# Performance work log

Hardware: AMD Instinct MI355X
Metric: run time of the kernel (lower is better)

## Reference

```python
import jax, jax.numpy as jnp
import numpy as np
import math

N_VERT = 35709
N_FACE = 70789
BATCH = 32


def _normalize(x, axis=-1, eps=1e-12):
    n = jnp.linalg.norm(x, axis=axis, keepdims=True)
    return x / jnp.maximum(n, eps)


def setup_inputs() -> dict:
    key = jax.random.key(0)
    ks = jax.random.split(key, 9)
    coeff = jax.random.normal(ks[0], (BATCH, 277), jnp.float32)
    idBase = jax.random.normal(ks[1], (3 * N_VERT, 80), jnp.float32)
    exBase = jax.random.normal(ks[2], (3 * N_VERT, 64), jnp.float32)
    texBase = jax.random.normal(ks[3], (3 * N_VERT, 100), jnp.float32)
    meanshape = jax.random.normal(ks[4], (3 * N_VERT,), jnp.float32)
    meantex = jax.random.normal(ks[5], (3 * N_VERT,), jnp.float32)
    face_buf = jax.random.randint(ks[6], (N_FACE, 3), 0, N_VERT, jnp.int32)
    # point_buf may index the appended zero-normal row at position N_FACE (padding)
    point_buf = jax.random.randint(ks[7], (N_VERT, 8), 0, N_FACE + 1, jnp.int32)
    keypoints = jax.random.randint(ks[8], (68,), 0, N_VERT, jnp.int32)
    return dict(coeff=coeff, idBase=idBase, exBase=exBase, texBase=texBase,
                meanshape=meanshape, meantex=meantex, face_buf=face_buf,
                point_buf=point_buf, keypoints=keypoints)


def reference(coeff, idBase, exBase, texBase, meanshape, meantex,
              face_buf, point_buf, keypoints):
    B = coeff.shape[0]
    # ---- Split_coeff (canonical 80/64/100/3/27/3 layout) ----
    id_c = coeff[:, :80]
    ex_c = coeff[:, 80:144]
    tex_c = coeff[:, 144:244]
    angles = coeff[:, 244:247]
    gamma = coeff[:, 247:274]
    trans = coeff[:, 274:277]
    cam_scale = jnp.ones((B, 1), coeff.dtype)
    f_scale = jnp.ones((B, 1), coeff.dtype)

    # ---- Shape formation ----
    fs = (jnp.einsum('ij,aj->ai', idBase, id_c)
          + jnp.einsum('ij,aj->ai', exBase, ex_c)
          + meanshape[None, :])
    fs = fs.reshape(B, -1, 3)  # [B, N, 3]
    fs = fs - jnp.mean(meanshape.reshape(-1, 3), axis=0)[None, None, :]

    # ---- Texture formation ----
    tex = (jnp.einsum('ij,aj->ai', texBase, tex_c) + meantex[None, :]).reshape(B, -1, 3)

    # ---- Rotation matrix (Rz @ Ry @ Rx, then transpose) ----
    cx, sx = jnp.cos(angles[:, 0]), jnp.sin(angles[:, 0])
    cy, sy = jnp.cos(angles[:, 1]), jnp.sin(angles[:, 1])
    cz, sz = jnp.cos(angles[:, 2]), jnp.sin(angles[:, 2])
    o, z = jnp.ones_like(cx), jnp.zeros_like(cx)
    Rx = jnp.stack([o, z, z, z, cx, -sx, z, sx, cx], -1).reshape(B, 3, 3)
    Ry = jnp.stack([cy, z, sy, z, o, z, -sy, z, cy], -1).reshape(B, 3, 3)
    Rz = jnp.stack([cz, -sz, z, sz, cz, z, z, z, o], -1).reshape(B, 3, 3)
    rot = jnp.swapaxes(jnp.matmul(jnp.matmul(Rz, Ry), Rx), 1, 2)  # [B,3,3]

    # ---- Compute_norm: gather face verts, cross, aggregate to vertices ----
    v1 = fs[:, face_buf[:, 0], :]  # [B, F, 3]
    v2 = fs[:, face_buf[:, 1], :]
    v3 = fs[:, face_buf[:, 2], :]
    face_norm = _normalize(jnp.cross(v1 - v2, v2 - v3), axis=2)  # [B, F, 3]
    face_norm = jnp.concatenate(
        [face_norm, jnp.zeros((B, 1, 3), face_norm.dtype)], axis=1)  # pad row
    v_norm = _normalize(jnp.sum(face_norm[:, point_buf, :], axis=2), axis=2)  # [B,N,3]

    norm_r = jnp.matmul(v_norm, rot)

    # ---- Rigid transform + landmarks ----
    fst = jnp.matmul(fs, rot) + trans[:, None, :]
    lm = fst[:, keypoints, :]  # [B, 68, 3]

    # ---- Projection block (applied to landmarks) ----
    focal = 1015.0 * f_scale  # [B,1]
    camera_pos = jnp.array([0.0, 0.0, 10.0], coeff.dtype) * cam_scale[:, :, None]  # [B,1,3]
    reverse_z = jnp.diag(jnp.array([1.0, 1.0, -1.0], coeff.dtype))
    z1 = jnp.zeros((B, 1), coeff.dtype)
    z2 = jnp.zeros((B, 2), coeff.dtype)
    o1 = jnp.ones((B, 1), coeff.dtype)
    p_matrix = jnp.concatenate(
        [focal, z1, 112.0 * o1, z1, focal, 112.0 * o1, z2, o1], axis=1).reshape(B, 3, 3)
    lm_cam = jnp.matmul(lm, reverse_z[None]) + camera_pos
    aug = jnp.matmul(lm_cam, jnp.swapaxes(p_matrix, 1, 2))
    landmark_p = aug[..., :2] / aug[..., 2:3]

    # ---- SH illumination ----
    init_lit = jnp.array([0.8, 0, 0, 0, 0, 0, 0, 0, 0], coeff.dtype)
    g = gamma.reshape(B, 3, 9) + init_lit[None, None, :]
    pi = math.pi
    a0, a1, a2 = pi, 2 * pi / math.sqrt(3.0), 2 * pi / math.sqrt(8.0)
    c0 = 1.0 / math.sqrt(4 * pi)
    c1 = math.sqrt(3.0) / math.sqrt(4 * pi)
    c2 = 3 * math.sqrt(5.0) / math.sqrt(12 * pi)
    nx, ny, nz = norm_r[..., 0], norm_r[..., 1], norm_r[..., 2]
    Y = jnp.stack([
        a0 * c0 * jnp.ones_like(nx),
        -a1 * c1 * ny,
        a1 * c1 * nz,
        -a1 * c1 * nx,
        a2 * c2 * nx * ny,
        -a2 * c2 * ny * nz,
        a2 * c2 * 0.5 / math.sqrt(3.0) * (3 * nz * nz - 1),
        -a2 * c2 * nx * nz,
        a2 * c2 * 0.5 * (nx * nx - ny * ny),
    ], axis=-1)  # [B, N, 9]
    lighting = jnp.einsum('bnk,bck->bnc', Y, g)  # [B, N, 3]
    face_color = tex * lighting

    return face_color, landmark_p, fst
```

## Files before the change

### kernel.cpp

```cpp
#include <hip/hip_runtime.h>

#define N_VERT 35709
#define N_FACE 70789
#define NB 32
#define M3 (3*N_VERT)

#define WS_FS4X  ((size_t)0)
#define WS_FN4X  (WS_FS4X + (size_t)N_VERT*128)
#define WS_CPAD  (WS_FN4X + (size_t)(N_FACE+1)*128)
#define WS_ROT   (WS_CPAD + (size_t)NB*256)
#define WS_TRE   (WS_ROT + (size_t)NB*9)
#define WS_G     (WS_TRE + (size_t)NB*3)
#define WS_MEAN  (WS_G + (size_t)NB*27)

#define FC_OFF   ((size_t)0)
#define LM_OFF   ((size_t)NB*M3)
#define FST_OFF  (LM_OFF + (size_t)NB*68*2)

#define A0C0 0.88622692545275801f
#define A1C1 1.77245385090551603f
#define A2C2 2.42703239430f
#define Y6C  0.70062393935f
#define Y8C  1.21351619715f

__global__ void __launch_bounds__(256) face3d_stageA1(
    const float* __restrict__ ms, float* __restrict__ ws) {
  float s0=0.f, s1=0.f, s2=0.f;
  for (int v = blockIdx.x*256 + threadIdx.x; v < N_VERT; v += gridDim.x*256) {
    s0 += ms[3*v+0]; s1 += ms[3*v+1]; s2 += ms[3*v+2];
  }
  #pragma unroll
  for (int off = 32; off > 0; off >>= 1) {
    s0 += __shfl_down(s0, off);
    s1 += __shfl_down(s1, off);
    s2 += __shfl_down(s2, off);
  }
  if ((threadIdx.x & 63) == 0) {
    atomicAdd(&ws[WS_MEAN+0], s0);
    atomicAdd(&ws[WS_MEAN+1], s1);
    atomicAdd(&ws[WS_MEAN+2], s2);
  }
}

__global__ void __launch_bounds__(256) face3d_stageA2(
    const float* __restrict__ coeff, float* __restrict__ ws) {
  int t = threadIdx.x;
  float m0 = ws[WS_MEAN+0]*(1.0f/N_VERT);
  float m1 = ws[WS_MEAN+1]*(1.0f/N_VERT);
  float m2 = ws[WS_MEAN+2]*(1.0f/N_VERT);
  float4* cp4 = (float4*)(ws + WS_CPAD);
  for (int idx = t; idx < 64*32; idx += 256) {
    int s4 = idx >> 5, b = idx & 31;
    int k = 4*s4;
    float4 v;
    v.x = (k < 244) ? coeff[b*277 + k + 0] : 0.f;
    v.y = (k < 244) ? coeff[b*277 + k + 1] : 0.f;
    v.z = (k < 244) ? coeff[b*277 + k + 2] : 0.f;
    v.w = (k < 244) ? coeff[b*277 + k + 3] : 0.f;
    cp4[idx] = v;
  }
  for (int idx = t; idx < NB*27; idx += 256) {
    int b = idx / 27, k = idx - b*27;
    ws[WS_G + idx] = coeff[b*277 + 247 + k] + (((k % 9) == 0) ? 0.8f : 0.0f);
  }
  if (t < NB) {
    int b = t;
    float ax = coeff[b*277+244], ay = coeff[b*277+245], az = coeff[b*277+246];
    float cx=cosf(ax), sx=sinf(ax);
    float cy=cosf(ay), sy=sinf(ay);
    float cz=cosf(az), sz=sinf(az);
    float T00=cz*cy, T01=-sz, T02=cz*sy;
    float T10=sz*cy, T11=cz,  T12=sz*sy;
    float T20=-sy,   T21=0.f, T22=cy;
    float R[3][3];
    R[0][0]=T00; R[0][1]=T01*cx+T02*sx; R[0][2]=-T01*sx+T02*cx;
    R[1][0]=T10; R[1][1]=T11*cx+T12*sx; R[1][2]=-T11*sx+T12*cx;
    R[2][0]=T20; R[2][1]=T21*cx+T22*sx; R[2][2]=-T21*sx+T22*cx;
    float rot[3][3];
    #pragma unroll
    for (int c=0;c<3;c++)
      #pragma unroll
      for (int j=0;j<3;j++)
        rot[c][j] = R[j][c];
    #pragma unroll
    for (int c=0;c<3;c++)
      #pragma unroll
      for (int j=0;j<3;j++)
        ws[WS_ROT + b*9 + c*3 + j] = rot[c][j];
    #pragma unroll
    for (int j=0;j<3;j++)
      ws[WS_TRE + b*3 + j] = coeff[b*277+274+j]
        - (m0*rot[0][j] + m1*rot[1][j] + m2*rot[2][j]);
  }
}


template<int NK4, int SOFF>
__device__ __forceinline__ void phaseKs(const float4* __restrict__ A,
                                        const float4* __restrict__ W,
                                        float* __restrict__ acc) {
  float4 cur = A[0];
  #pragma unroll 1
  for (int s = 0; s < NK4; ++s) {
    float4 a = cur;
    if (s + 1 < NK4) cur = A[s+1];
    const float4* __restrict__ Ws = W + (size_t)(SOFF + s)*32;
    #pragma unroll
    for (int b = 0; b < NB; ++b) {
      float4 w = Ws[b];
      acc[b] = fmaf(a.w, w.w, fmaf(a.z, w.z, fmaf(a.y, w.y, fmaf(a.x, w.x, acc[b]))));
    }
  }
}

__global__ void __launch_bounds__(256) face3d_stageB(
    const float* __restrict__ idB, const float* __restrict__ exB,
    const float* __restrict__ texB, const float* __restrict__ meanshape,
    const float* __restrict__ meantex, const float* __restrict__ cpadT,
    float* __restrict__ fs4x, float* __restrict__ texOut) {
  int t = threadIdx.x;
  int bid = blockIdx.x;
  int isTex = bid & 1;
  int r = (bid >> 1)*256 + t;
  if (r >= M3) return;
  const float4* __restrict__ W = (const float4*)cpadT;

  float acc[NB];
  #pragma unroll
  for (int b = 0; b < NB; ++b) acc[b] = 0.f;

  if (!isTex) {
    phaseKs<20, 0 >((const float4*)idB + (size_t)r*20, W, acc);
    phaseKs<16, 20>((const float4*)exB + (size_t)r*16, W, acc);
    float msv = meanshape[r];
    int v = r/3, c = r - 3*v;
    float* dst = fs4x + (size_t)v*128 + c;
    #pragma unroll
    for (int b = 0; b < NB; ++b) dst[b*4] = acc[b] + msv;
  } else {
    phaseKs<25, 36>((const float4*)texB + (size_t)r*25, W, acc);
    float mtv = meantex[r];
    #pragma unroll
    for (int b = 0; b < NB; ++b) texOut[(size_t)b*M3 + r] = acc[b] + mtv;
  }
}

__global__ void __launch_bounds__(256) face3d_stageC(
    const int* __restrict__ face_buf, const float* __restrict__ fs4x,
    float* __restrict__ fn4x) {
  int t = threadIdx.x;
  int b = t & 31, fi = t >> 5;
  int f = blockIdx.x*8 + fi;
  if (f > N_FACE) return;
  float4* o = (float4*)(fn4x + ((size_t)f*32 + b)*4);
  if (f == N_FACE) { *o = make_float4(0.f,0.f,0.f,0.f); return; }
  int i0 = face_buf[f*3+0];
  int i1 = face_buf[f*3+1];
  int i2 = face_buf[f*3+2];
  float4 p1 = *(const float4*)(fs4x + ((size_t)i0*32 + b)*4);
  float4 p2 = *(const float4*)(fs4x + ((size_t)i1*32 + b)*4);
  float4 p3 = *(const float4*)(fs4x + ((size_t)i2*32 + b)*4);
  float e1x = p1.x-p2.x, e1y = p1.y-p2.y, e1z = p1.z-p2.z;
  float e2x = p2.x-p3.x, e2y = p2.y-p3.y, e2z = p2.z-p3.z;
  float nx = e1y*e2z - e1z*e2y;
  float ny = e1z*e2x - e1x*e2z;
  float nz = e1x*e2y - e1y*e2x;
  float inv = 1.0f / fmaxf(sqrtf(nx*nx + ny*ny + nz*nz), 1e-12f);
  *o = make_float4(nx*inv, ny*inv, nz*inv, 0.f);
}

__global__ void __launch_bounds__(256) face3d_stageD(
    const int* __restrict__ point_buf, const int* __restrict__ keypoints,
    const float* __restrict__ fs4x, const float* __restrict__ fn4x,
    const float* __restrict__ rotAll, const float* __restrict__ treAll,
    const float* __restrict__ gAll, float* __restrict__ out) {
  const int mainBlocks = (N_VERT + 7)/8;
  int bid = blockIdx.x;
  int t = threadIdx.x;
  if (bid < mainBlocks) {
    __shared__ float rotL[NB*9];
    __shared__ float treL[NB*3];
    __shared__ float gL[NB*27];
    __shared__ float fstL[NB*33];
    __shared__ float LL[NB*33];
    if (t < NB*9)  rotL[t] = rotAll[t];
    if (t < NB*3)  treL[t] = treAll[t];
    for (int i = t; i < NB*27; i += 256) gL[i] = gAll[i];
    __syncthreads();
    int b = t & 31, vi = t >> 5;
    int v0 = bid*8;
    int v = v0 + vi;
    if (v < N_VERT) {
      const int4 pb0 = *(const int4*)(point_buf + (size_t)v*8);
      const int4 pb1 = *(const int4*)(point_buf + (size_t)v*8 + 4);
      float4 g0 = *(const float4*)(fn4x + ((size_t)pb0.x*32 + b)*4);
      float4 g1 = *(const float4*)(fn4x + ((size_t)pb0.y*32 + b)*4);
      float4 g2 = *(const float4*)(fn4x + ((size_t)pb0.z*32 + b)*4);
      float4 g3 = *(const float4*)(fn4x + ((size_t)pb0.w*32 + b)*4);
      float4 g4 = *(const float4*)(fn4x + ((size_t)pb1.x*32 + b)*4);
      float4 g5 = *(const float4*)(fn4x + ((size_t)pb1.y*32 + b)*4);
      float4 g6 = *(const float4*)(fn4x + ((size_t)pb1.z*32 + b)*4);
      float4 g7 = *(const float4*)(fn4x + ((size_t)pb1.w*32 + b)*4);
      float sx = ((g0.x+g1.x)+(g2.x+g3.x)) + ((g4.x+g5.x)+(g6.x+g7.x));
      float sy = ((g0.y+g1.y)+(g2.y+g3.y)) + ((g4.y+g5.y)+(g6.y+g7.y));
      float sz = ((g0.z+g1.z)+(g2.z+g3.z)) + ((g4.z+g5.z)+(g6.z+g7.z));
      float inv = 1.0f / fmaxf(sqrtf(sx*sx + sy*sy + sz*sz), 1e-12f);
      float n0 = sx*inv, n1 = sy*inv, n2 = sz*inv;
      const float* rot = rotL + b*9;
      float r00=rot[0], r01=rot[1], r02=rot[2];
      float r10=rot[3], r11=rot[4], r12=rot[5];
      float r20=rot[6], r21=rot[7], r22=rot[8];
      float nx = n0*r00 + n1*r10 + n2*r20;
      float ny = n0*r01 + n1*r11 + n2*r21;
      float nz = n0*r02 + n1*r12 + n2*r22;
      float Y1 = -A1C1*ny;
      float Y2 =  A1C1*nz;
      float Y3 = -A1C1*nx;
      float Y4 =  A2C2*nx*ny;
      float Y5 = -A2C2*ny*nz;
      float Y6 =  Y6C*(3.f*nz*nz - 1.f);
      float Y7 = -A2C2*nx*nz;
      float Y8 =  Y8C*(nx*nx - ny*ny);
      const float* g = gL + b*27;
      #pragma unroll
      for (int c = 0; c < 3; ++c) {
        const float* gc = g + c*9;
        float Lc = A0C0*gc[0] + Y1*gc[1] + Y2*gc[2] + Y3*gc[3] + Y4*gc[4]
                 + Y5*gc[5] + Y6*gc[6] + Y7*gc[7] + Y8*gc[8];
        LL[b*33 + vi*4 + c] = Lc;
      }
      float4 fsv = *(const float4*)(fs4x + ((size_t)v*32 + b)*4);
      const float* tre = treL + b*3;
      fstL[b*33 + vi*4 + 0] = fsv.x*r00 + fsv.y*r10 + fsv.z*r20 + tre[0];
      fstL[b*33 + vi*4 + 1] = fsv.x*r01 + fsv.y*r11 + fsv.z*r21 + tre[1];
      fstL[b*33 + vi*4 + 2] = fsv.x*r02 + fsv.y*r12 + fsv.z*r22 + tre[2];
    }
    __syncthreads();
    int b2 = t >> 3, w = t & 7;
    if (v0 + w < N_VERT) {
      size_t obase = (size_t)b2*M3 + (size_t)(v0 + w)*3;
      float f0 = fstL[b2*33 + w*4 + 0];
      float f1 = fstL[b2*33 + w*4 + 1];
      float f2 = fstL[b2*33 + w*4 + 2];
      out[FST_OFF + obase + 0] = f0;
      out[FST_OFF + obase + 1] = f1;
      out[FST_OFF + obase + 2] = f2;
      float l0 = LL[b2*33 + w*4 + 0];
      float l1 = LL[b2*33 + w*4 + 1];
      float l2 = LL[b2*33 + w*4 + 2];
      float t0 = out[FC_OFF + obase + 0];
      float t1 = out[FC_OFF + obase + 1];
      float t2 = out[FC_OFF + obase + 2];
      out[FC_OFF + obase + 0] = t0*l0;
      out[FC_OFF + obase + 1] = t1*l1;
      out[FC_OFF + obase + 2] = t2*l2;
    }
  } else {
    int idx = (bid - mainBlocks)*256 + t;
    if (idx >= NB*68) return;
    int b = idx & 31, j = idx >> 5;
    int kp = keypoints[j];
    const float* rot = rotAll + b*9;
    const float* tre = treAll + b*3;
    float4 fsv = *(const float4*)(fs4x + ((size_t)kp*32 + b)*4);
    float o0 = fsv.x*rot[0] + fsv.y*rot[3] + fsv.z*rot[6] + tre[0];
    float o1 = fsv.x*rot[1] + fsv.y*rot[4] + fsv.z*rot[7] + tre[1];
    float o2 = fsv.x*rot[2] + fsv.y*rot[5] + fsv.z*rot[8] + tre[2];
    float zc = 10.0f - o2;
    float axv = 1015.0f*o0 + 112.0f*zc;
    float ayv = 1015.0f*o1 + 112.0f*zc;
    out[LM_OFF + (size_t)b*136 + (size_t)j*2 + 0] = axv/zc;
    out[LM_OFF + (size_t)b*136 + (size_t)j*2 + 1] = ayv/zc;
  }
}

extern "C" void kernel_launch(void* const* d_in, const int* in_sizes, int n_in,
                              void* d_out, int out_size, void* d_ws, size_t ws_size,
                              hipStream_t stream) {
  const float* coeff     = (const float*)d_in[0];
  const float* idB       = (const float*)d_in[1];
  const float* exB       = (const float*)d_in[2];
  const float* texB      = (const float*)d_in[3];
  const float* meanshape = (const float*)d_in[4];
  const float* meantex   = (const float*)d_in[5];
  const int*   face_buf  = (const int*)d_in[6];
  const int*   point_buf = (const int*)d_in[7];
  const int*   keypoints = (const int*)d_in[8];
  float* out = (float*)d_out;
  float* ws  = (float*)d_ws;

  hipMemsetAsync((char*)d_ws + WS_MEAN*sizeof(float), 0, 3*sizeof(float), stream);

  hipLaunchKernelGGL(face3d_stageA1, dim3(56), dim3(256), 0, stream, meanshape, ws);
  hipLaunchKernelGGL(face3d_stageA2, dim3(1), dim3(256), 0, stream, coeff, ws);

  int gridB = 2 * ((M3 + 255)/256);
  hipLaunchKernelGGL(face3d_stageB, dim3(gridB), dim3(256), 0, stream,
                     idB, exB, texB, meanshape, meantex,
                     ws + WS_CPAD, ws + WS_FS4X, out + FC_OFF);

  int gridC = (N_FACE + 1 + 7)/8;
  hipLaunchKernelGGL(face3d_stageC, dim3(gridC), dim3(256), 0, stream,
                     face_buf, ws + WS_FS4X, ws + WS_FN4X);

  int mainBlocks = (N_VERT + 7)/8;
  int lmBlocks   = (NB*68 + 255)/256;
  hipLaunchKernelGGL(face3d_stageD, dim3(mainBlocks + lmBlocks), dim3(256), 0, stream,
                     point_buf, keypoints, ws + WS_FS4X, ws + WS_FN4X,
                     ws + WS_ROT, ws + WS_TRE, ws + WS_G, out);
}
```

Measured before the change: 291.5 us.

## Stage coefficient weights in LDS and compute two rows per thread in stageB

The basis GEMM kernel now copies the per-batch coefficient matrix into shared memory once per block. Each thread computes two output rows, so every loaded weight float4 feeds twice as many FMAs. Blocks shrink to 128 threads while each block still covers 256 rows. This cuts repeated global/L1 reads of the coefficients, at the cost of twice the accumulator registers (64 floats), which may lower occupancy. The two rows a thread handles sit 128 apart, so each row is still read with its own strided loads.

```diff
diff --git a/kernel.cpp b/kernel.cpp
--- a/kernel.cpp
+++ b/kernel.cpp
@@ -96,52 +96,84 @@
 
 
 template<int NK4, int SOFF>
-__device__ __forceinline__ void phaseKs(const float4* __restrict__ A,
-                                        const float4* __restrict__ W,
-                                        float* __restrict__ acc) {
-  float4 cur = A[0];
+__device__ __forceinline__ void gemm2(const float4* __restrict__ A0,
+                                      const float4* __restrict__ A1,
+                                      const float4* __restrict__ Wl,
+                                      float acc[2][NB]) {
+  float4 c0 = A0[0], c1 = A1[0];
   #pragma unroll 1
   for (int s = 0; s < NK4; ++s) {
-    float4 a = cur;
-    if (s + 1 < NK4) cur = A[s+1];
-    const float4* __restrict__ Ws = W + (size_t)(SOFF + s)*32;
+    float4 a0 = c0, a1 = c1;
+    if (s + 1 < NK4) { c0 = A0[s+1]; c1 = A1[s+1]; }
+    const float4* __restrict__ Ws = Wl + (size_t)(SOFF + s)*32;
     #pragma unroll
     for (int b = 0; b < NB; ++b) {
       float4 w = Ws[b];
-      acc[b] = fmaf(a.w, w.w, fmaf(a.z, w.z, fmaf(a.y, w.y, fmaf(a.x, w.x, acc[b]))));
-    }
-  }
-}
-
-__global__ void __launch_bounds__(256) face3d_stageB(
+      acc[0][b] = fmaf(a0.w, w.w, fmaf(a0.z, w.z, fmaf(a0.y, w.y, fmaf(a0.x, w.x, acc[0][b]))));
+      acc[1][b] = fmaf(a1.w, w.w, fmaf(a1.z, w.z, fmaf(a1.y, w.y, fmaf(a1.x, w.x, acc[1][b]))));
+    }
+  }
+}
+
+__global__ void __launch_bounds__(128) face3d_stageB(
     const float* __restrict__ idB, const float* __restrict__ exB,
     const float* __restrict__ texB, const float* __restrict__ meanshape,
     const float* __restrict__ meantex, const float* __restrict__ cpadT,
     float* __restrict__ fs4x, float* __restrict__ texOut) {
+  __shared__ float4 Wl[36*32];
   int t = threadIdx.x;
   int bid = blockIdx.x;
   int isTex = bid & 1;
-  int r = (bid >> 1)*256 + t;
-  if (r >= M3) return;
-  const float4* __restrict__ W = (const float4*)cpadT;
-
-  float acc[NB];
+  int r0 = (bid >> 1) * 256;
+
+  const float4* __restrict__ cp4 = (const float4*)cpadT;
+  if (!isTex) {
+    #pragma unroll
+    for (int i = 0; i < 9; ++i) Wl[t + 128*i] = cp4[t + 128*i];
+  } else {
+    for (int i = t; i < 25*32; i += 128) Wl[i] = cp4[36*32 + i];
+  }
+  __syncthreads();
+
+  int ra = r0 + t;
+  int rb = r0 + t + 128;
+  int rac = (ra < M3) ? ra : (M3-1);
+  int rbc = (rb < M3) ? rb : (M3-1);
+
+  float acc[2][NB];
   #pragma unroll
-  for (int b = 0; b < NB; ++b) acc[b] = 0.f;
+  for (int j = 0; j < 2; ++j)
+    #pragma unroll
+    for (int b = 0; b < NB; ++b) acc[j][b] = 0.f;
 
   if (!isTex) {
-    phaseKs<20, 0 >((const float4*)idB + (size_t)r*20, W, acc);
-    phaseKs<16, 20>((const float4*)exB + (size_t)r*16, W, acc);
-    float msv = meanshape[r];
-    int v = r/3, c = r - 3*v;
-    float* dst = fs4x + (size_t)v*128 + c;
-    #pragma unroll
-    for (int b = 0; b < NB; ++b) dst[b*4] = acc[b] + msv;
+    gemm2<20, 0 >((const float4*)idB + (size_t)rac*20,
+                  (const float4*)idB + (size_t)rbc*20, Wl, acc);
+    gemm2<16, 20>((const float4*)exB + (size_t)rac*16,
+                  (const float4*)exB + (size_t)rbc*16, Wl, acc);
+    #pragma unroll
+    for (int j = 0; j < 2; ++j) {
+      int r = (j == 0) ? ra : rb;
+      if (r < M3) {
+        float msv = meanshape[r];
+        int v = r/3, c = r - 3*v;
+        float* dst = fs4x + (size_t)v*128 + c;
+        #pragma unroll
+        for (int b = 0; b < NB; ++b) dst[b*4] = acc[j][b] + msv;
+      }
+    }
   } else {
-    phaseKs<25, 36>((const float4*)texB + (size_t)r*25, W, acc);
-    float mtv = meantex[r];
-    #pragma unroll
-    for (int b = 0; b < NB; ++b) texOut[(size_t)b*M3 + r] = acc[b] + mtv;
+    gemm2<25, 0 >((const float4*)texB + (size_t)rac*25,
+                  (const float4*)texB + (size_t)rbc*25, Wl, acc);
+    #pragma unroll
+    for (int j = 0; j < 2; ++j) {
+      int r = (j == 0) ? ra : rb;
+      if (r < M3) {
+        float mtv = meantex[r];
+        #pragma unroll
+        for (int b = 0; b < NB; ++b) texOut[(size_t)b*M3 + r] = acc[j][b] + mtv;
+      }
+    }
   }
 }
 
@@ -295,7 +327,7 @@
   hipLaunchKernelGGL(face3d_stageA2, dim3(1), dim3(256), 0, stream, coeff, ws);
 
   int gridB = 2 * ((M3 + 255)/256);
-  hipLaunchKernelGGL(face3d_stageB, dim3(gridB), dim3(256), 0, stream,
+  hipLaunchKernelGGL(face3d_stageB, dim3(gridB), dim3(128), 0, stream,
                      idB, exB, texB, meanshape, meantex,
                      ws + WS_CPAD, ws + WS_FS4X, out + FC_OFF);
 
```

Result: faster. 278.2 us (-4.6%).
